# Performance work log

Hardware: AMD Instinct MI355X
Metric: run time of the kernel (lower is better)

Reference implementation:

```python
import jax, jax.numpy as jnp
import numpy as np

B, S, D, H = 4, 2048, 1024, 16
DK = D // H


def setup_inputs() -> dict:
    key = jax.random.key(0)
    ks = jax.random.split(key, 7)
    xq = jax.random.normal(ks[0], (B, S, D), dtype=jnp.float32)
    xk = jax.random.normal(ks[1], (B, S, D), dtype=jnp.float32)
    xv = jax.random.normal(ks[2], (B, S, D), dtype=jnp.float32)
    attention_mask = jnp.ones((B, S), dtype=jnp.int32)  # all-valid padding mask
    scale = 0.02
    Wq = jax.random.normal(ks[3], (D, D), dtype=jnp.float32) * scale
    Wk = jax.random.normal(ks[4], (D, D), dtype=jnp.float32) * scale
    Wv = jax.random.normal(ks[5], (D, D), dtype=jnp.float32) * scale
    Wo = jax.random.normal(ks[6], (D, D), dtype=jnp.float32) * scale
    return {"x_query": xq, "x_key": xk, "x_value": xv,
            "attention_mask": attention_mask,
            "Wq": Wq, "Wk": Wk, "Wv": Wv, "Wo": Wo}


def reference(x_query, x_key, x_value, attention_mask, Wq, Wk, Wv, Wo):
    b, sq, d = x_query.shape
    sk = x_key.shape[1]
    # nn.Linear(bias=False): y = x @ W.T
    Q = x_query @ Wq.T
    K = x_key @ Wk.T
    V = x_value @ Wv.T
    # torch .split(dk, dim=-1) -> contiguous head slices == reshape (B,S,H,DK)
    Qh = Q.reshape(b, sq, H, DK).transpose(0, 2, 1, 3)  # (B,H,Sq,DK)
    Kh = K.reshape(b, sk, H, DK).transpose(0, 2, 1, 3)
    Vh = V.reshape(b, sk, H, DK).transpose(0, 2, 1, 3)
    scores = jnp.einsum('bhqd,bhkd->bhqk', Qh, Kh) / jnp.sqrt(
        jnp.asarray(DK, dtype=Qh.dtype))
    # causal mask (mask_future=True)
    causal = jnp.tril(jnp.ones((sq, sk), dtype=bool))
    scores = jnp.where(causal[None, None, :, :], scores, -jnp.inf)
    # padding mask (B,Sk) -> (B,1,1,Sk)
    pad = (attention_mask != 0)[:, None, None, :]
    scores = jnp.where(pad, scores, -jnp.inf)
    attn = jax.nn.softmax(scores, axis=-1)
    out = jnp.einsum('bhqk,bhkd->bhqd', attn, Vh)  # (B,H,Sq,DK)
    out = out.transpose(0, 2, 1, 3).reshape(b, sq, d)
    return out @ Wo.T
```

## Files before the change

### kernel.cpp

```cpp
#include <hip/hip_runtime.h>
#include <stdint.h>

#define BB 4
#define SS 2048
#define DD 1024
#define HH 16
#define DKK 64

typedef unsigned short u16;
typedef short s16x8 __attribute__((ext_vector_type(8)));
typedef float f32x4 __attribute__((ext_vector_type(4)));

__device__ __forceinline__ void async_copy16(const void* g, void* l) {
  __builtin_amdgcn_global_load_lds(
      (const __attribute__((address_space(1))) void*)g,
      (__attribute__((address_space(3))) void*)l, 16, 0, 0);
}

__device__ __forceinline__ u16 f2bf(float f) {
  union { float f; uint32_t u; } x; x.f = f;
  uint32_t r = x.u + 0x7fffu + ((x.u >> 16) & 1u);
  return (u16)(r >> 16);
}

__global__ __launch_bounds__(256) void cvt_kernel(
    const float* __restrict__ x0, const float* __restrict__ x1,
    const float* __restrict__ x2, const float* __restrict__ w0,
    const float* __restrict__ w1, const float* __restrict__ w2,
    const float* __restrict__ w3, u16* __restrict__ dst) {
  const size_t base = ((size_t)blockIdx.x * 256 + threadIdx.x) * 8;
  const float* src;
  size_t off;
  if (base < 25165824ull) {
    const size_t t = base >> 23;
    src = (t == 0) ? x0 : (t == 1) ? x1 : x2;
    off = base & 8388607ull;
  } else {
    const size_t r = base - 25165824ull;
    const size_t t = r >> 20;
    src = (t == 0) ? w0 : (t == 1) ? w1 : (t == 2) ? w2 : w3;
    off = r & 1048575ull;
  }
  const float4 a = *(const float4*)(src + off);
  const float4 b = *(const float4*)(src + off + 4);
  s16x8 o;
  o[0] = (short)f2bf(a.x); o[1] = (short)f2bf(a.y);
  o[2] = (short)f2bf(a.z); o[3] = (short)f2bf(a.w);
  o[4] = (short)f2bf(b.x); o[5] = (short)f2bf(b.y);
  o[6] = (short)f2bf(b.z); o[7] = (short)f2bf(b.w);
  *(s16x8*)(dst + base) = o;
}

template <bool IN_F32, bool OUT_F32>
__global__ __launch_bounds__(256, 3) void gemm_bt(
    const void* __restrict__ Ap, const void* __restrict__ Bp, void* __restrict__ Cp,
    size_t asegstride, size_t bsegstride, size_t csegstride, int vt_seg) {
  const int K = 1024, N = 1024;
  __shared__ u16 Alds[128 * 64];
  __shared__ u16 Blds[128 * 64];
  const int tid = threadIdx.x;
  const int wid = tid >> 6, lane = tid & 63;
  const int quad = lane >> 4, l16 = lane & 15;
  const int mtile = blockIdx.x >> 3;
  const int ntile = blockIdx.x & 7;
  const int wm = wid >> 1, wn = wid & 1;
  const int seg = blockIdx.y;
  f32x4 acc[4][4] = {};
  for (int kb = 0; kb < K; kb += 64) {
    if constexpr (IN_F32) {
      const float* Af = (const float*)Ap + seg * asegstride + (size_t)mtile * 128 * K;
      const float* Bf = (const float*)Bp + seg * bsegstride + (size_t)ntile * 128 * K;
#pragma unroll
      for (int i = 0; i < 8; ++i) {
        const int c = i * 256 + tid;
        const int row = c >> 4, g = c & 15;
        const int cc = g >> 1, h = g & 1;
        const int sl = row * 8 + (cc ^ (row & 7));
        {
          const float4 v = *(const float4*)(Af + (size_t)row * K + kb + g * 4);
          ushort4 o;
          o.x = f2bf(v.x); o.y = f2bf(v.y); o.z = f2bf(v.z); o.w = f2bf(v.w);
          *(ushort4*)&Alds[sl * 8 + h * 4] = o;
        }
        {
          const float4 v = *(const float4*)(Bf + (size_t)row * K + kb + g * 4);
          ushort4 o;
          o.x = f2bf(v.x); o.y = f2bf(v.y); o.z = f2bf(v.z); o.w = f2bf(v.w);
          *(ushort4*)&Blds[sl * 8 + h * 4] = o;
        }
      }
    } else {
      const u16* Ab = (const u16*)Ap + seg * asegstride + (size_t)mtile * 128 * K;
      const u16* Bb = (const u16*)Bp + seg * bsegstride + (size_t)ntile * 128 * K;
#pragma unroll
      for (int i = 0; i < 4; ++i) {
        const int s = i * 256 + tid;
        const int row = s >> 3;
        const int cc = (s & 7) ^ (row & 7);
        async_copy16(Ab + (size_t)row * K + kb + cc * 8,
                     (char*)Alds + (i * 256 + wid * 64) * 16);
        async_copy16(Bb + (size_t)row * K + kb + cc * 8,
                     (char*)Blds + (i * 256 + wid * 64) * 16);
      }
    }
    __syncthreads();
#pragma unroll
    for (int ks = 0; ks < 2; ++ks) {
      s16x8 af[4], bfr[4];
#pragma unroll
      for (int i = 0; i < 4; ++i) {
        const int R = wm * 64 + i * 16 + l16;
        af[i] = *(const s16x8*)&Alds[(R * 8 + ((ks * 4 + quad) ^ (l16 & 7))) * 8];
      }
#pragma unroll
      for (int j = 0; j < 4; ++j) {
        const int R = wn * 64 + j * 16 + l16;
        bfr[j] = *(const s16x8*)&Blds[(R * 8 + ((ks * 4 + quad) ^ (l16 & 7))) * 8];
      }
#pragma unroll
      for (int i = 0; i < 4; ++i)
#pragma unroll
        for (int j = 0; j < 4; ++j)
          acc[i][j] = __builtin_amdgcn_mfma_f32_16x16x32_bf16(af[i], bfr[j], acc[i][j], 0, 0, 0);
    }
    __syncthreads();
  }
  const int row0 = mtile * 128 + wm * 64 + quad * 4;
  const int col0 = ntile * 128 + wn * 64 + l16;
  if (seg == vt_seg) {
    u16* VT = (u16*)Cp + (size_t)seg * csegstride;
#pragma unroll
    for (int i = 0; i < 4; ++i)
#pragma unroll
      for (int j = 0; j < 4; ++j) {
        const int col = col0 + j * 16;
        const int row = row0 + i * 16;
        const int bb = row >> 11, s0 = row & 2047;
        const size_t dst = (((size_t)bb * HH + (col >> 6)) * DKK + (col & 63)) * SS + s0;
        ushort4 o;
        o.x = f2bf(acc[i][j][0]); o.y = f2bf(acc[i][j][1]);
        o.z = f2bf(acc[i][j][2]); o.w = f2bf(acc[i][j][3]);
        *(ushort4*)((u16*)Cp + (size_t)seg * csegstride + dst - (size_t)seg * csegstride + (size_t)seg * csegstride) = o;
        *(ushort4*)(VT + dst) = o;
      }
  } else {
#pragma unroll
    for (int i = 0; i < 4; ++i)
#pragma unroll
      for (int j = 0; j < 4; ++j)
#pragma unroll
        for (int r = 0; r < 4; ++r) {
          const size_t idx = (size_t)(row0 + i * 16 + r) * N + col0 + j * 16;
          if constexpr (OUT_F32) ((float*)Cp)[seg * csegstride + idx] = acc[i][j][r];
          else                   ((u16*)Cp)[seg * csegstride + idx] = f2bf(acc[i][j][r]);
        }
  }
}

__global__ __launch_bounds__(256, 3) void attn_kernel(
    const u16* __restrict__ Q, const u16* __restrict__ K, const u16* __restrict__ VT,
    const int* __restrict__ mask, u16* __restrict__ O) {
  __shared__ u16 Klds[64 * 64];
  __shared__ u16 Vt[64 * 64];
  __shared__ u16 Plds[128 * 64];
  __shared__ float bias[64];
  const int bid = blockIdx.x;
  const int qt = 15 - (bid >> 6);
  const int b = (bid >> 4) & 3;
  const int h = bid & 15;
  const int tid = threadIdx.x;
  const int wid = tid >> 6, lane = tid & 63;
  const int quad = lane >> 4, l16 = lane & 15;
  const int q0 = qt * 128;
  const u16* Qb = Q + ((size_t)b * SS + q0) * DD + h * DKK;
  const u16* Kb0 = K + (size_t)b * SS * DD + h * DKK;
  const u16* VTb = VT + ((size_t)(b * HH + h)) * DKK * SS;
  s16x8 qf[2][2];
#pragma unroll
  for (int rg = 0; rg < 2; ++rg)
#pragma unroll
    for (int ks = 0; ks < 2; ++ks)
      qf[rg][ks] = *(const s16x8*)(Qb + (size_t)(wid * 32 + rg * 16 + l16) * DD +
                                   ks * 32 + quad * 8);
  s16x8 onesf;
#pragma unroll
  for (int i = 0; i < 8; ++i) onesf[i] = (short)0x3F80;
  f32x4 oacc[2][4] = {};
  f32x4 lacc[2] = {};
  const int ktiles = 2 * qt + 2;
  for (int kt = 0; kt < ktiles; ++kt) {
    const u16* Kb = Kb0 + (size_t)(kt * 64) * DD;
#pragma unroll
    for (int i = 0; i < 2; ++i) {
      const int s = i * 256 + tid;
      const int row = s >> 3;
      const int cc = (s & 7) ^ (row & 7);
      async_copy16(Kb + (size_t)row * DD + cc * 8,
                   (char*)Klds + (i * 256 + wid * 64) * 16);
    }
#pragma unroll
    for (int i = 0; i < 2; ++i) {
      const int s = i * 256 + tid;
      const int row = s >> 3;
      const int cc = (s & 7) ^ (row & 7);
      async_copy16(VTb + (size_t)row * SS + kt * 64 + cc * 8,
                   (char*)Vt + ((i * 256 + wid * 64) * 16));
    }
    if (tid < 64) bias[tid] = mask[(size_t)b * SS + kt * 64 + tid] ? 0.0f : -1e30f;
    __syncthreads();
    float biasj[4];
#pragma unroll
    for (int j = 0; j < 4; ++j) biasj[j] = bias[j * 16 + l16];
    f32x4 sacc[2][4] = {};
#pragma unroll
    for (int ks = 0; ks < 2; ++ks) {
      s16x8 kf[4];
#pragma unroll
      for (int j = 0; j < 4; ++j) {
        const int R = j * 16 + l16;
        kf[j] = *(const s16x8*)&Klds[(R * 8 + ((ks * 4 + quad) ^ (l16 & 7))) * 8];
      }
#pragma unroll
      for (int rg = 0; rg < 2; ++rg)
#pragma unroll
        for (int j = 0; j < 4; ++j)
          sacc[rg][j] = __builtin_amdgcn_mfma_f32_16x16x32_bf16(qf[rg][ks], kf[j],
                                                               sacc[rg][j], 0, 0, 0);
    }
    const bool causal = (kt >= 2 * qt);
#pragma unroll
    for (int rg = 0; rg < 2; ++rg)
#pragma unroll
      for (int r = 0; r < 4; ++r) {
        const int qrow = q0 + wid * 32 + rg * 16 + quad * 4 + r;
#pragma unroll
        for (int j = 0; j < 4; ++j) {
          float p = __expf(sacc[rg][j][r] * 0.125f + biasj[j]);
          if (causal && (kt * 64 + j * 16 + l16) > qrow) p = 0.0f;
          Plds[(wid * 32 + rg * 16 + quad * 4 + r) * 64 + ((j ^ quad) * 16 + l16)] =
              f2bf(p);
        }
      }
    asm volatile("s_waitcnt lgkmcnt(0)" ::: "memory");
    const int swz = (l16 >> 2) & 3;
#pragma unroll
    for (int ks = 0; ks < 2; ++ks) {
      const int jr = ks * 2 + (quad >> 1);
      s16x8 pf[2];
#pragma unroll
      for (int rg = 0; rg < 2; ++rg)
        pf[rg] = *(const s16x8*)&Plds[(wid * 32 + rg * 16 + l16) * 64 +
                                      ((jr ^ swz) * 16 + (quad & 1) * 8)];
#pragma unroll
      for (int jt = 0; jt < 4; ++jt) {
        const int d = jt * 16 + l16;
        const s16x8 vf = *(const s16x8*)&Vt[(d * 8 + ((ks * 4 + quad) ^ (d & 7))) * 8];
#pragma unroll
        for (int rg = 0; rg < 2; ++rg)
          oacc[rg][jt] = __builtin_amdgcn_mfma_f32_16x16x32_bf16(pf[rg], vf,
                                                                oacc[rg][jt], 0, 0, 0);
      }
#pragma unroll
      for (int rg = 0; rg < 2; ++rg)
        lacc[rg] = __builtin_amdgcn_mfma_f32_16x16x32_bf16(pf[rg], onesf, lacc[rg],
                                                           0, 0, 0);
    }
    __syncthreads();
  }
  u16* Ob = O + ((size_t)b * SS + q0) * DD + h * DKK;
#pragma unroll
  for (int rg = 0; rg < 2; ++rg)
#pragma unroll
    for (int r = 0; r < 4; ++r) {
      const float inv = 1.0f / lacc[rg][r];
      const int row = wid * 32 + rg * 16 + quad * 4 + r;
#pragma unroll
      for (int jt = 0; jt < 4; ++jt)
        Ob[(size_t)row * DD + jt * 16 + l16] = f2bf(oacc[rg][jt][r] * inv);
    }
}

extern "C" void kernel_launch(void* const* d_in, const int* in_sizes, int n_in,
                              void* d_out, int out_size, void* d_ws, size_t ws_size,
                              hipStream_t stream) {
  const float* xq = (const float*)d_in[0];
  const float* xk = (const float*)d_in[1];
  const float* xv = (const float*)d_in[2];
  const int* mask = (const int*)d_in[3];
  const float* Wq = (const float*)d_in[4];
  const float* Wk = (const float*)d_in[5];
  const float* Wv = (const float*)d_in[6];
  const float* Wo = (const float*)d_in[7];
  float* out = (float*)d_out;
  const size_t elems = (size_t)BB * SS * DD;
  const size_t welems = (size_t)DD * DD;
  if (ws_size >= 109051904ull) {
    u16* wsb = (u16*)d_ws;
    u16* Xq = wsb;
    u16* Wqb = wsb + 3 * elems;
    u16* Wob = Wqb + 3 * welems;
    u16* Qb = wsb + 3 * elems + 4 * welems;
    u16* Kb = Qb + elems;
    u16* Vb = Kb + elems;
    u16* Ob = wsb;
    cvt_kernel<<<14336, 256, 0, stream>>>(xq, xk, xv, Wq, Wk, Wv, Wo, wsb);
    gemm_bt<false, false><<<dim3(512, 3), 256, 0, stream>>>(
        Xq, Wqb, Qb, elems, welems, elems, 2);
    attn_kernel<<<BB * HH * (SS / 128), 256, 0, stream>>>(Qb, Kb, Vb, mask, Ob);
    gemm_bt<false, true><<<dim3(512, 1), 256, 0, stream>>>(Ob, Wob, out, 0, 0, 0, -1);
  } else {
    u16* Qb = (u16*)d_ws;
    u16* Kb = Qb + elems;
    u16* Vb = Kb + elems;
    u16* Ob = Vb + elems;
    gemm_bt<true, false><<<dim3(512, 1), 256, 0, stream>>>(xq, Wq, Qb, 0, 0, 0, -1);
    gemm_bt<true, false><<<dim3(512, 1), 256, 0, stream>>>(xk, Wk, Kb, 0, 0, 0, -1);
    gemm_bt<true, false><<<dim3(512, 1), 256, 0, stream>>>(xv, Wv, Vb, 0, 0, 0, 0);
    attn_kernel<<<BB * HH * (SS / 128), 256, 0, stream>>>(Qb, Kb, Vb, mask, Ob);
    gemm_bt<false, true><<<dim3(512, 1), 256, 0, stream>>>(Ob, Wo, out, 0, 0, 0, -1);
  }
}
```

Before: 319.1 us.

## Double-buffer K/V tiles in attention with async prefetch and manual waitcnt

The attention loop now double-buffers K and V in LDS, issuing the async global-to-LDS loads for the next tile before computing the current one, and uses a vmcnt-based wait plus raw s_barrier instead of __syncthreads. The padding mask is read straight into registers instead of going through a shared bias array, and MFMA sections are given raised wave priority. It also drops a redundant duplicate store in the VT write path of the GEMM epilogue. The goal is to hide global load latency behind MFMA work, at the cost of twice the K/V LDS footprint, which may lower occupancy, and fragile hand-written wait counts.

```diff
diff --git a/kernel.cpp b/kernel.cpp
--- a/kernel.cpp
+++ b/kernel.cpp
@@ -140,7 +140,6 @@
         ushort4 o;
         o.x = f2bf(acc[i][j][0]); o.y = f2bf(acc[i][j][1]);
         o.z = f2bf(acc[i][j][2]); o.w = f2bf(acc[i][j][3]);
-        *(ushort4*)((u16*)Cp + (size_t)seg * csegstride + dst - (size_t)seg * csegstride + (size_t)seg * csegstride) = o;
         *(ushort4*)(VT + dst) = o;
       }
   } else {
@@ -160,10 +159,9 @@
 __global__ __launch_bounds__(256, 3) void attn_kernel(
     const u16* __restrict__ Q, const u16* __restrict__ K, const u16* __restrict__ VT,
     const int* __restrict__ mask, u16* __restrict__ O) {
-  __shared__ u16 Klds[64 * 64];
-  __shared__ u16 Vt[64 * 64];
+  __shared__ u16 Klds[2][64 * 64];
+  __shared__ u16 Vt[2][64 * 64];
   __shared__ u16 Plds[128 * 64];
-  __shared__ float bias[64];
   const int bid = blockIdx.x;
   const int qt = 15 - (bid >> 6);
   const int b = (bid >> 4) & 3;
@@ -175,6 +173,7 @@
   const u16* Qb = Q + ((size_t)b * SS + q0) * DD + h * DKK;
   const u16* Kb0 = K + (size_t)b * SS * DD + h * DKK;
   const u16* VTb = VT + ((size_t)(b * HH + h)) * DKK * SS;
+  const int* mrow = mask + (size_t)b * SS;
   s16x8 qf[2][2];
 #pragma unroll
   for (int rg = 0; rg < 2; ++rg)
@@ -188,15 +187,15 @@
   f32x4 oacc[2][4] = {};
   f32x4 lacc[2] = {};
   const int ktiles = 2 * qt + 2;
-  for (int kt = 0; kt < ktiles; ++kt) {
-    const u16* Kb = Kb0 + (size_t)(kt * 64) * DD;
+
+  auto stage = [&](int bufsel, int kt) {
 #pragma unroll
     for (int i = 0; i < 2; ++i) {
       const int s = i * 256 + tid;
       const int row = s >> 3;
       const int cc = (s & 7) ^ (row & 7);
-      async_copy16(Kb + (size_t)row * DD + cc * 8,
-                   (char*)Klds + (i * 256 + wid * 64) * 16);
+      async_copy16(Kb0 + (size_t)(kt * 64 + row) * DD + cc * 8,
+                   (char*)(&Klds[bufsel][0]) + (i * 256 + wid * 64) * 16);
     }
 #pragma unroll
     for (int i = 0; i < 2; ++i) {
@@ -204,21 +203,35 @@
       const int row = s >> 3;
       const int cc = (s & 7) ^ (row & 7);
       async_copy16(VTb + (size_t)row * SS + kt * 64 + cc * 8,
-                   (char*)Vt + ((i * 256 + wid * 64) * 16));
-    }
-    if (tid < 64) bias[tid] = mask[(size_t)b * SS + kt * 64 + tid] ? 0.0f : -1e30f;
-    __syncthreads();
+                   (char*)(&Vt[bufsel][0]) + (i * 256 + wid * 64) * 16);
+    }
+  };
+
+  stage(0, 0);
+  for (int kt = 0; kt < ktiles; ++kt) {
+    const int cur = kt & 1;
+    int mv[4];
+#pragma unroll
+    for (int j = 0; j < 4; ++j) mv[j] = mrow[kt * 64 + j * 16 + l16];
+    __builtin_amdgcn_sched_barrier(0);
+    const bool have_next = (kt + 1 < ktiles);
+    if (have_next) stage(cur ^ 1, kt + 1);
+    __builtin_amdgcn_sched_barrier(0);
+    if (have_next) asm volatile("s_waitcnt vmcnt(4)\n\ts_barrier" ::: "memory");
+    else           asm volatile("s_waitcnt vmcnt(0)\n\ts_barrier" ::: "memory");
+
     float biasj[4];
 #pragma unroll
-    for (int j = 0; j < 4; ++j) biasj[j] = bias[j * 16 + l16];
+    for (int j = 0; j < 4; ++j) biasj[j] = mv[j] ? 0.0f : -1e30f;
     f32x4 sacc[2][4] = {};
+    __builtin_amdgcn_s_setprio(1);
 #pragma unroll
     for (int ks = 0; ks < 2; ++ks) {
       s16x8 kf[4];
 #pragma unroll
       for (int j = 0; j < 4; ++j) {
         const int R = j * 16 + l16;
-        kf[j] = *(const s16x8*)&Klds[(R * 8 + ((ks * 4 + quad) ^ (l16 & 7))) * 8];
+        kf[j] = *(const s16x8*)&Klds[cur][(R * 8 + ((ks * 4 + quad) ^ (l16 & 7))) * 8];
       }
 #pragma unroll
       for (int rg = 0; rg < 2; ++rg)
@@ -227,6 +240,7 @@
           sacc[rg][j] = __builtin_amdgcn_mfma_f32_16x16x32_bf16(qf[rg][ks], kf[j],
                                                                sacc[rg][j], 0, 0, 0);
     }
+    __builtin_amdgcn_s_setprio(0);
     const bool causal = (kt >= 2 * qt);
 #pragma unroll
     for (int rg = 0; rg < 2; ++rg)
@@ -243,6 +257,7 @@
       }
     asm volatile("s_waitcnt lgkmcnt(0)" ::: "memory");
     const int swz = (l16 >> 2) & 3;
+    __builtin_amdgcn_s_setprio(1);
 #pragma unroll
     for (int ks = 0; ks < 2; ++ks) {
       const int jr = ks * 2 + (quad >> 1);
@@ -254,7 +269,7 @@
 #pragma unroll
       for (int jt = 0; jt < 4; ++jt) {
         const int d = jt * 16 + l16;
-        const s16x8 vf = *(const s16x8*)&Vt[(d * 8 + ((ks * 4 + quad) ^ (d & 7))) * 8];
+        const s16x8 vf = *(const s16x8*)&Vt[cur][(d * 8 + ((ks * 4 + quad) ^ (d & 7))) * 8];
 #pragma unroll
         for (int rg = 0; rg < 2; ++rg)
           oacc[rg][jt] = __builtin_amdgcn_mfma_f32_16x16x32_bf16(pf[rg], vf,
@@ -265,7 +280,8 @@
         lacc[rg] = __builtin_amdgcn_mfma_f32_16x16x32_bf16(pf[rg], onesf, lacc[rg],
                                                            0, 0, 0);
     }
-    __syncthreads();
+    __builtin_amdgcn_s_setprio(0);
+    asm volatile("s_barrier" ::: "memory");
   }
   u16* Ob = O + ((size_t)b * SS + q0) * DD + h * DKK;
 #pragma unroll
```

After: 325.9 us. 2.1% more time.

## Keep attention probabilities in registers via transposed MFMA and cross-lane shuffles

Applied to the files above, without the earlier changes.

Computes S^T by swapping the MFMA operands so each lane holds consecutive key columns. The probabilities are then packed to bf16 with v_cvt_pk_bf16_f32 and rearranged into the PV A-operand layout using ds_swizzle and ds_bpermute, instead of a round trip through the Plds shared buffer. Exp uses exp2 with the log2e-folded scale, and launch bounds rise to 4 blocks per SM now that LDS use is smaller. A redundant duplicate VT store in the GEMM epilogue is removed. The cost is extra lane permutes and selects plus possible register pressure at the higher occupancy target.

```diff
diff --git a/kernel.cpp b/kernel.cpp
--- a/kernel.cpp
+++ b/kernel.cpp
@@ -21,6 +21,16 @@
   union { float f; uint32_t u; } x; x.f = f;
   uint32_t r = x.u + 0x7fffu + ((x.u >> 16) & 1u);
   return (u16)(r >> 16);
+}
+
+__device__ __forceinline__ uint32_t cvtpk(float a, float b) {
+  uint32_t d;
+  asm("v_cvt_pk_bf16_f32 %0, %1, %2" : "=v"(d) : "v"(a), "v"(b));
+  return d;
+}
+
+__device__ __forceinline__ uint32_t swz16(uint32_t x) {
+  return (uint32_t)__builtin_amdgcn_ds_swizzle((int)x, 0x401F);
 }
 
 __global__ __launch_bounds__(256) void cvt_kernel(
@@ -140,7 +150,6 @@
         ushort4 o;
         o.x = f2bf(acc[i][j][0]); o.y = f2bf(acc[i][j][1]);
         o.z = f2bf(acc[i][j][2]); o.w = f2bf(acc[i][j][3]);
-        *(ushort4*)((u16*)Cp + (size_t)seg * csegstride + dst - (size_t)seg * csegstride + (size_t)seg * csegstride) = o;
         *(ushort4*)(VT + dst) = o;
       }
   } else {
@@ -157,12 +166,11 @@
   }
 }
 
-__global__ __launch_bounds__(256, 3) void attn_kernel(
+__global__ __launch_bounds__(256, 4) void attn_kernel(
     const u16* __restrict__ Q, const u16* __restrict__ K, const u16* __restrict__ VT,
     const int* __restrict__ mask, u16* __restrict__ O) {
   __shared__ u16 Klds[64 * 64];
   __shared__ u16 Vt[64 * 64];
-  __shared__ u16 Plds[128 * 64];
   __shared__ float bias[64];
   const int bid = blockIdx.x;
   const int qt = 15 - (bid >> 6);
@@ -187,6 +195,18 @@
   for (int i = 0; i < 8; ++i) onesf[i] = (short)0x3F80;
   f32x4 oacc[2][4] = {};
   f32x4 lacc[2] = {};
+  const float c_scale = 0.18033688f;
+  const bool qodd = (quad & 1) != 0;
+  const bool is_hi = (lane >= 32);
+  const bool midq = (quad == 1) || (quad == 2);
+  const int xaddr = (lane ^ 32) << 2;
+  const int qrow0 = q0 + wid * 32 + l16;
+  auto mixf = [&](uint32_t vj0, uint32_t vj1) -> uint32_t {
+    const uint32_t S  = is_hi ? vj1 : vj0;
+    const uint32_t S2 = is_hi ? vj0 : vj1;
+    const uint32_t R  = (uint32_t)__builtin_amdgcn_ds_bpermute(xaddr, (int)S2);
+    return midq ? R : S;
+  };
   const int ktiles = 2 * qt + 2;
   for (int kt = 0; kt < ktiles; ++kt) {
     const u16* Kb = Kb0 + (size_t)(kt * 64) * DD;
@@ -208,10 +228,10 @@
     }
     if (tid < 64) bias[tid] = mask[(size_t)b * SS + kt * 64 + tid] ? 0.0f : -1e30f;
     __syncthreads();
-    float biasj[4];
-#pragma unroll
-    for (int j = 0; j < 4; ++j) biasj[j] = bias[j * 16 + l16];
-    f32x4 sacc[2][4] = {};
+    f32x4 bj[4];
+#pragma unroll
+    for (int j = 0; j < 4; ++j) bj[j] = *(const f32x4*)&bias[j * 16 + quad * 4];
+    f32x4 st[2][4] = {};
 #pragma unroll
     for (int ks = 0; ks < 2; ++ks) {
       s16x8 kf[4];
@@ -224,33 +244,48 @@
       for (int rg = 0; rg < 2; ++rg)
 #pragma unroll
         for (int j = 0; j < 4; ++j)
-          sacc[rg][j] = __builtin_amdgcn_mfma_f32_16x16x32_bf16(qf[rg][ks], kf[j],
-                                                               sacc[rg][j], 0, 0, 0);
+          st[rg][j] = __builtin_amdgcn_mfma_f32_16x16x32_bf16(kf[j], qf[rg][ks],
+                                                              st[rg][j], 0, 0, 0);
     }
     const bool causal = (kt >= 2 * qt);
-#pragma unroll
-    for (int rg = 0; rg < 2; ++rg)
-#pragma unroll
-      for (int r = 0; r < 4; ++r) {
-        const int qrow = q0 + wid * 32 + rg * 16 + quad * 4 + r;
-#pragma unroll
-        for (int j = 0; j < 4; ++j) {
-          float p = __expf(sacc[rg][j][r] * 0.125f + biasj[j]);
-          if (causal && (kt * 64 + j * 16 + l16) > qrow) p = 0.0f;
-          Plds[(wid * 32 + rg * 16 + quad * 4 + r) * 64 + ((j ^ quad) * 16 + l16)] =
-              f2bf(p);
+    uint32_t pkv[2][8];
+#pragma unroll
+    for (int rg = 0; rg < 2; ++rg) {
+      const int qrow = qrow0 + rg * 16;
+#pragma unroll
+      for (int j = 0; j < 4; ++j) {
+        float p[4];
+#pragma unroll
+        for (int r = 0; r < 4; ++r) {
+          float v = __builtin_amdgcn_exp2f(st[rg][j][r] * c_scale + bj[j][r]);
+          if (causal && (kt * 64 + j * 16 + quad * 4 + r) > qrow) v = 0.0f;
+          p[r] = v;
         }
-      }
-    asm volatile("s_waitcnt lgkmcnt(0)" ::: "memory");
-    const int swz = (l16 >> 2) & 3;
+        pkv[rg][j * 2 + 0] = cvtpk(p[0], p[1]);
+        pkv[rg][j * 2 + 1] = cvtpk(p[2], p[3]);
+      }
+    }
 #pragma unroll
     for (int ks = 0; ks < 2; ++ks) {
-      const int jr = ks * 2 + (quad >> 1);
+      const int j0 = ks * 2, j1 = ks * 2 + 1;
       s16x8 pf[2];
 #pragma unroll
-      for (int rg = 0; rg < 2; ++rg)
-        pf[rg] = *(const s16x8*)&Plds[(wid * 32 + rg * 16 + l16) * 64 +
-                                      ((jr ^ swz) * 16 + (quad & 1) * 8)];
+      for (int rg = 0; rg < 2; ++rg) {
+        const uint32_t Xa0 = pkv[rg][j0 * 2 + 0], Xa1 = pkv[rg][j0 * 2 + 1];
+        const uint32_t Xb0 = pkv[rg][j1 * 2 + 0], Xb1 = pkv[rg][j1 * 2 + 1];
+        const uint32_t Pa0 = swz16(Xa0), Pa1 = swz16(Xa1);
+        const uint32_t Pb0 = swz16(Xb0), Pb1 = swz16(Xb1);
+        const uint32_t Ea0 = qodd ? Pa0 : Xa0, Oa0 = qodd ? Xa0 : Pa0;
+        const uint32_t Ea1 = qodd ? Pa1 : Xa1, Oa1 = qodd ? Xa1 : Pa1;
+        const uint32_t Eb0 = qodd ? Pb0 : Xb0, Ob0 = qodd ? Xb0 : Pb0;
+        const uint32_t Eb1 = qodd ? Pb1 : Xb1, Ob1 = qodd ? Xb1 : Pb1;
+        union { uint32_t w[4]; s16x8 v; } u;
+        u.w[0] = mixf(Ea0, Eb0);
+        u.w[1] = mixf(Ea1, Eb1);
+        u.w[2] = mixf(Oa0, Ob0);
+        u.w[3] = mixf(Oa1, Ob1);
+        pf[rg] = u.v;
+      }
 #pragma unroll
       for (int jt = 0; jt < 4; ++jt) {
         const int d = jt * 16 + l16;
```

Measured after the change: 318.4 us. Within noise of the previous version (-0.2%).
